# Optimization experiments

Hardware: AMD Instinct MI355X
Metric: run time of the kernel (lower is better)

## Reference

```python
import jax, jax.numpy as jnp
import numpy as np
import math

B, C, L_MIX, L_REF = 4, 512, 2048, 2048
NUM_HEADS = 8
HEAD_DIM = C // NUM_HEADS
MAX_LEN = 5000
EPS = 1e-5


def layer_norm(x, gamma, beta):
    mu = jnp.mean(x, axis=-1, keepdims=True)
    var = jnp.mean(jnp.square(x - mu), axis=-1, keepdims=True)
    return (x - mu) * jax.lax.rsqrt(var + EPS) * gamma + beta


def setup_inputs() -> dict:
    key = jax.random.key(0)
    ks = jax.random.split(key, 12)
    inp = {
        "query": jax.random.normal(ks[0], (B, C, L_MIX), dtype=jnp.float32),
        "key_value": jax.random.normal(ks[1], (B, C, L_REF), dtype=jnp.float32),
        "pos_encoding": jax.random.normal(ks[2], (1, MAX_LEN, C), dtype=jnp.float32) * 0.01,
        "q_gamma": jnp.ones((C,), jnp.float32),
        "q_beta": jnp.zeros((C,), jnp.float32),
        "k_gamma": jnp.ones((C,), jnp.float32),
        "k_beta": jnp.zeros((C,), jnp.float32),
        "Wq": jax.random.normal(ks[3], (C, C), jnp.float32) / math.sqrt(C),
        "bq": jax.random.normal(ks[4], (C,), jnp.float32) * 0.01,
        "Wk": jax.random.normal(ks[5], (C, C), jnp.float32) / math.sqrt(C),
        "bk": jax.random.normal(ks[6], (C,), jnp.float32) * 0.01,
        "Wv": jax.random.normal(ks[7], (C, C), jnp.float32) / math.sqrt(C),
        "bv": jax.random.normal(ks[8], (C,), jnp.float32) * 0.01,
        "Wo": jax.random.normal(ks[9], (C, C), jnp.float32) / math.sqrt(C),
        "bo": jax.random.normal(ks[10], (C,), jnp.float32) * 0.01,
    }
    return inp


def reference(query, key_value, pos_encoding, q_gamma, q_beta, k_gamma, k_beta,
              Wq, bq, Wk, bk, Wv, bv, Wo, bo):
    # (B, C, L) -> (B, L, C)
    q = jnp.transpose(query, (0, 2, 1))
    kv = jnp.transpose(key_value, (0, 2, 1))
    Lm, Lr = q.shape[1], kv.shape[1]
    q = q + pos_encoding[:, :Lm, :]
    kv = kv + pos_encoding[:, :Lr, :]
    q = layer_norm(q, q_gamma, q_beta)
    kv = layer_norm(kv, k_gamma, k_beta)
    Q = q @ Wq + bq          # (B, Lm, C)
    K = kv @ Wk + bk         # (B, Lr, C)
    V = kv @ Wv + bv         # (B, Lr, C)
    Q = Q.reshape(B, Lm, NUM_HEADS, HEAD_DIM)
    K = K.reshape(B, Lr, NUM_HEADS, HEAD_DIM)
    V = V.reshape(B, Lr, NUM_HEADS, HEAD_DIM)
    scale = math.sqrt(HEAD_DIM)
    scores = jnp.einsum('bqhd,bkhd->bhqk', Q, K) / scale  # (B, H, Lm, Lr)
    scores = jnp.clip(scores, -50.0, 50.0)
    attn = jax.nn.softmax(scores, axis=-1)  # dropout is identity at eval
    out = jnp.einsum('bhqk,bkhd->bqhd', attn, V).reshape(B, Lm, C)
    out = out @ Wo + bo
    out = out + q            # residual with normed/pos-encoded query, per source
    return jnp.transpose(out, (0, 2, 1))  # (B, C, Lm)
```

## Files before the change

### kernel.cpp

```cpp
#include <hip/hip_runtime.h>
#include <hip/hip_bf16.h>

#define B_ 4
#define C_ 512
#define L_ 2048
#define H_ 8
#define D_ 64
#define EPS_ 1e-5f

using short8 = __attribute__((ext_vector_type(8))) short;
using s4v    = __attribute__((ext_vector_type(4))) short;
using f32x4  = __attribute__((ext_vector_type(4))) float;

#if defined(__has_builtin)
#if __has_builtin(__builtin_amdgcn_exp2f)
#define EXP2(x) __builtin_amdgcn_exp2f(x)
#else
#define EXP2(x) exp2f(x)
#endif
#else
#define EXP2(x) exp2f(x)
#endif

#define GLOAD_LDS16(g, l)                                                     \
  __builtin_amdgcn_global_load_lds(                                           \
      (const __attribute__((address_space(1))) void*)(g),                     \
      (__attribute__((address_space(3))) void*)(l), 16, 0, 0)

static __device__ __forceinline__ short f2bf(float f) {
  __hip_bfloat16 h = __float2bfloat16(f);
  return __builtin_bit_cast(short, h);
}
static __device__ __forceinline__ float bf2f(short s) {
  return __bfloat162float(__builtin_bit_cast(__hip_bfloat16, s));
}

__global__ __launch_bounds__(256) void k_pre(
    const float* __restrict__ Wq, const float* __restrict__ Wk,
    const float* __restrict__ Wv, const float* __restrict__ Wo,
    short* __restrict__ Wt,
    const float* __restrict__ query, const float* __restrict__ kv,
    const float* __restrict__ pos,
    const float* __restrict__ qg, const float* __restrict__ qb,
    const float* __restrict__ kg, const float* __restrict__ kb,
    short* __restrict__ qn, short* __restrict__ kvn) {
  __shared__ alignas(16) float SB[16 * 516 + 32];
  int t = threadIdx.x;
  int id = blockIdx.x;

  if (id < 1024) {
    int m = id >> 8, rest = id & 255;
    int k0 = (rest >> 4) * 32, n0 = (rest & 15) * 32;
    const float* W = (m == 0) ? Wq : (m == 1) ? Wk : (m == 2) ? Wv : Wo;
    float (*T)[33] = (float(*)[33])SB;
    {
      int kl = t >> 3, n4 = (t & 7) * 4;
      float4 v = *(const float4*)(W + (size_t)(k0 + kl) * C_ + n0 + n4);
      T[kl][n4] = v.x; T[kl][n4 + 1] = v.y; T[kl][n4 + 2] = v.z; T[kl][n4 + 3] = v.w;
    }
    __syncthreads();
    {
      int nl = t >> 3, k4 = (t & 7) * 4;
      s4v o;
#pragma unroll
      for (int j = 0; j < 4; ++j) o[j] = f2bf(T[k4 + j][nl]);
      *(s4v*)(Wt + (size_t)(m * C_ + n0 + nl) * C_ + k0 + k4) = o;
    }
    return;
  }

  id -= 1024;
  int z  = id >> 9;
  int b  = (id >> 7) & 3;
  int l0 = (id & 127) * 16;
  const float* src = z ? kv : query;
  const float* g   = z ? kg : qg;
  const float* be  = z ? kb : qb;
  short* dst       = z ? kvn : qn;

  float (*T)[516] = (float(*)[516])SB;
  float* mu_s = SB + 16 * 516;
  float* rs_s = mu_s + 16;

#pragma unroll
  for (int i = 0; i < 8; ++i) {
    int idx = i * 256 + t;
    int cc = idx >> 2, lg = (idx & 3) * 4;
    float4 v = *(const float4*)(src + (size_t)(b * C_ + cc) * L_ + l0 + lg);
    T[lg + 0][cc] = v.x; T[lg + 1][cc] = v.y; T[lg + 2][cc] = v.z; T[lg + 3][cc] = v.w;
  }
  __syncthreads();
#pragma unroll
  for (int i = 0; i < 8; ++i) {
    int idx = i * 256 + t;
    int ll = idx >> 7, c4 = (idx & 127) * 4;
    float4 p = *(const float4*)(pos + (size_t)(l0 + ll) * C_ + c4);
    float4* tp = (float4*)&T[ll][c4];
    float4 cur = *tp;
    cur.x += p.x; cur.y += p.y; cur.z += p.z; cur.w += p.w;
    *tp = cur;
  }
  __syncthreads();
  {
    int row = t >> 4, j = t & 15;
    float s1 = 0.f, s2 = 0.f;
    for (int c = j; c < C_; c += 16) { float v = T[row][c]; s1 += v; s2 += v * v; }
    for (int m = 1; m < 16; m <<= 1) {
      s1 += __shfl_xor(s1, m, 64);
      s2 += __shfl_xor(s2, m, 64);
    }
    if (j == 0) {
      float mu  = s1 * (1.0f / C_);
      float var = s2 * (1.0f / C_) - mu * mu;
      mu_s[row] = mu;
      rs_s[row] = rsqrtf(var + EPS_);
    }
  }
  __syncthreads();
#pragma unroll
  for (int i = 0; i < 8; ++i) {
    int idx = i * 256 + t;
    int ll = idx >> 7, c4 = (idx & 127) * 4;
    float4 v  = *(const float4*)&T[ll][c4];
    float4 gv = *(const float4*)(g + c4);
    float4 bv = *(const float4*)(be + c4);
    float mu = mu_s[ll], rs = rs_s[ll];
    s4v o;
    o[0] = f2bf((v.x - mu) * rs * gv.x + bv.x);
    o[1] = f2bf((v.y - mu) * rs * gv.y + bv.y);
    o[2] = f2bf((v.z - mu) * rs * gv.z + bv.z);
    o[3] = f2bf((v.w - mu) * rs * gv.w + bv.w);
    *(s4v*)(dst + (size_t)(b * L_ + l0 + ll) * C_ + c4) = o;
  }
}

__global__ __launch_bounds__(256) void k_gemm_qkv(
    const short* __restrict__ qn, const short* __restrict__ kvn,
    const short* __restrict__ Wt,
    const float* __restrict__ bq, const float* __restrict__ bk, const float* __restrict__ bv,
    short* __restrict__ Qw, short* __restrict__ Kw, short* __restrict__ Vtg) {
  int z = blockIdx.z;
  const short* X    = z ? kvn : qn;
  const short* W    = Wt + (size_t)z * C_ * C_;
  const float* bias = (z == 0) ? bq : (z == 1) ? bk : bv;
  float sc          = (z == 0) ? 0.18033688f : 1.0f;

  int m0 = blockIdx.x * 128, n0 = blockIdx.y * 128;
  __shared__ alignas(16) short As[128 * 64];
  __shared__ alignas(16) short Bs[128 * 64];
  int t = threadIdx.x, lane = t & 63, w = t >> 6;
  int wm = w & 1, wn = w >> 1;
  int quad = lane >> 4, c = lane & 15;

  const short* Ag = X + (size_t)(m0 + w * 32 + (lane >> 3)) * C_ + (lane & 7) * 8;
  const short* Bg = W + (size_t)(n0 + w * 32 + (lane >> 3)) * C_ + (lane & 7) * 8;

  f32x4 zero4 = {0.f, 0.f, 0.f, 0.f};
  f32x4 acc[4][4];
  for (int i = 0; i < 4; ++i) for (int j = 0; j < 4; ++j) acc[i][j] = zero4;

  for (int k0 = 0; k0 < C_; k0 += 64) {
    __syncthreads();
#pragma unroll
    for (int j = 0; j < 4; ++j) {
      GLOAD_LDS16(Ag + (size_t)(j * 8) * C_ + k0, As + (w * 32 + j * 8) * 64);
      GLOAD_LDS16(Bg + (size_t)(j * 8) * C_ + k0, Bs + (w * 32 + j * 8) * 64);
    }
    __syncthreads();
#pragma unroll
    for (int kc = 0; kc < 2; ++kc) {
      short8 a[4], bf[4];
#pragma unroll
      for (int i = 0; i < 4; ++i)
        a[i]  = *(const short8*)(As + (wm * 64 + i * 16 + c) * 64 + kc * 32 + quad * 8);
#pragma unroll
      for (int j = 0; j < 4; ++j)
        bf[j] = *(const short8*)(Bs + (wn * 64 + j * 16 + c) * 64 + kc * 32 + quad * 8);
#pragma unroll
      for (int i = 0; i < 4; ++i)
#pragma unroll
        for (int j = 0; j < 4; ++j)
          acc[i][j] = __builtin_amdgcn_mfma_f32_16x16x32_bf16(a[i], bf[j], acc[i][j], 0, 0, 0);
    }
  }

  if (z == 2) {
#pragma unroll
    for (int i = 0; i < 4; ++i)
#pragma unroll
      for (int j = 0; j < 4; ++j) {
        int colg = n0 + wn * 64 + j * 16 + c;
        float bia = bias[colg];
        int hh = colg >> 6, dd = colg & 63;
        int rowg = m0 + wm * 64 + i * 16 + quad * 4;
        int bb = rowg >> 11, l = rowg & (L_ - 1);
        s4v o;
#pragma unroll
        for (int r = 0; r < 4; ++r) o[r] = f2bf(acc[i][j][r] + bia);
        *(s4v*)(Vtg + ((size_t)(bb * H_ + hh) * D_ + dd) * L_ + l) = o;
      }
  } else {
    short* Y = (z == 0) ? Qw : Kw;
#pragma unroll
    for (int i = 0; i < 4; ++i)
#pragma unroll
      for (int j = 0; j < 4; ++j) {
        int colg = n0 + wn * 64 + j * 16 + c;
        float bia = bias[colg];
        int rowg = m0 + wm * 64 + i * 16 + quad * 4;
#pragma unroll
        for (int r = 0; r < 4; ++r)
          Y[(size_t)(rowg + r) * C_ + colg] = f2bf((acc[i][j][r] + bia) * sc);
      }
  }
}

#define LDP 72
#define LDC 68
__global__ __launch_bounds__(256, 2) void k_attn(
    const short* __restrict__ Qw, const short* __restrict__ Kw,
    const short* __restrict__ Vtg, short* __restrict__ Ow) {
  int bh = blockIdx.x & 31;
  int l0 = (blockIdx.x >> 5) * 128;
  int b = bh >> 3, h = bh & 7;
  __shared__ alignas(16) short Pw[4][16 * LDP];
  __shared__ alignas(16) float Cbuf[128 * LDC];
  __shared__ float Lbuf[128];
  int t = threadIdx.x, lane = t & 63, w = t >> 6;
  int qh = w & 1, ls = w >> 1;
  int quad = lane >> 4, c = lane & 15;

  short8 qa[4][2];
#pragma unroll
  for (int s = 0; s < 4; ++s) {
    const short* qp = Qw + ((size_t)(b * L_ + l0 + qh * 64 + s * 16 + c) * H_ + h) * D_ + quad * 8;
    qa[s][0] = *(const short8*)qp;
    qa[s][1] = *(const short8*)(qp + 32);
  }

  f32x4 zero4 = {0.f, 0.f, 0.f, 0.f};
  f32x4 acc[4][4];
#pragma unroll
  for (int s = 0; s < 4; ++s)
    for (int dt = 0; dt < 4; ++dt) acc[s][dt] = zero4;
  float lsum[4] = {0.f, 0.f, 0.f, 0.f};

  const short* Kb = Kw + ((size_t)(b * L_) * H_ + h) * D_;
  const short* Vb = Vtg + (size_t)(b * H_ + h) * D_ * L_;
  short* pb = &Pw[w][0];

  for (int lr0 = ls * 64; lr0 < L_; lr0 += 128) {
    short8 kf[4][2], vf[4][2];
#pragma unroll
    for (int T = 0; T < 4; ++T) {
      const short* kp = Kb + (size_t)(lr0 + T * 16 + c) * C_ + quad * 8;
      kf[T][0] = *(const short8*)kp;
      kf[T][1] = *(const short8*)(kp + 32);
    }
#pragma unroll
    for (int dt = 0; dt < 4; ++dt) {
      const short* vp = Vb + (size_t)(dt * 16 + c) * L_ + lr0 + quad * 8;
      vf[dt][0] = *(const short8*)vp;
      vf[dt][1] = *(const short8*)(vp + 32);
    }

#pragma unroll
    for (int s = 0; s < 4; ++s) {
      f32x4 st[4] = {zero4, zero4, zero4, zero4};
#pragma unroll
      for (int T = 0; T < 4; ++T) {
        st[T] = __builtin_amdgcn_mfma_f32_16x16x32_bf16(kf[T][0], qa[s][0], st[T], 0, 0, 0);
        st[T] = __builtin_amdgcn_mfma_f32_16x16x32_bf16(kf[T][1], qa[s][1], st[T], 0, 0, 0);
      }
#pragma unroll
      for (int T = 0; T < 4; ++T) {
        s4v pk;
#pragma unroll
        for (int r = 0; r < 4; ++r) {
          float p = EXP2(st[T][r]);
          lsum[s] += p;
          pk[r] = f2bf(p);
        }
        *(s4v*)(pb + c * LDP + T * 16 + quad * 4) = pk;
      }
#pragma unroll
      for (int hf = 0; hf < 2; ++hf) {
        short8 pf = *(const short8*)(pb + c * LDP + hf * 32 + quad * 8);
#pragma unroll
        for (int dt = 0; dt < 4; ++dt)
          acc[s][dt] = __builtin_amdgcn_mfma_f32_16x16x32_bf16(vf[dt][hf], pf, acc[s][dt], 0, 0, 0);
      }
    }
  }

#pragma unroll
  for (int s = 0; s < 4; ++s) {
    lsum[s] += __shfl_xor(lsum[s], 16, 64);
    lsum[s] += __shfl_xor(lsum[s], 32, 64);
  }

  if (ls == 1) {
#pragma unroll
    for (int s = 0; s < 4; ++s) {
      int q = qh * 64 + s * 16 + c;
#pragma unroll
      for (int dt = 0; dt < 4; ++dt)
        *(f32x4*)(Cbuf + q * LDC + dt * 16 + quad * 4) = acc[s][dt];
      if (quad == 0) Lbuf[q] = lsum[s];
    }
  }
  __syncthreads();
  if (ls == 0) {
#pragma unroll
    for (int s = 0; s < 4; ++s) {
      int q = qh * 64 + s * 16 + c;
      float inv = 1.0f / (lsum[s] + Lbuf[q]);
#pragma unroll
      for (int dt = 0; dt < 4; ++dt) {
        f32x4 o = *(const f32x4*)(Cbuf + q * LDC + dt * 16 + quad * 4);
        s4v ov;
#pragma unroll
        for (int r = 0; r < 4; ++r) ov[r] = f2bf((acc[s][dt][r] + o[r]) * inv);
        *(s4v*)(Ow + ((size_t)(b * L_ + l0 + q) * H_ + h) * D_ + dt * 16 + quad * 4) = ov;
      }
    }
  }
}

__global__ __launch_bounds__(256) void k_gemm_out(
    const short* __restrict__ Ow, const short* __restrict__ Wot,
    const float* __restrict__ bo, const short* __restrict__ qn,
    float* __restrict__ out) {
  int m0 = blockIdx.x * 128, n0 = blockIdx.y * 128;
  __shared__ alignas(16) short As[128 * 64];
  __shared__ alignas(16) short Bs[128 * 64];
  int t = threadIdx.x, lane = t & 63, w = t >> 6;
  int wm = w & 1, wn = w >> 1;
  int quad = lane >> 4, c = lane & 15;

  const short* Ag = Ow  + (size_t)(m0 + w * 32 + (lane >> 3)) * C_ + (lane & 7) * 8;
  const short* Bg = Wot + (size_t)(n0 + w * 32 + (lane >> 3)) * C_ + (lane & 7) * 8;

  f32x4 zero4 = {0.f, 0.f, 0.f, 0.f};
  f32x4 acc[4][4];
  for (int i = 0; i < 4; ++i) for (int j = 0; j < 4; ++j) acc[i][j] = zero4;

  for (int k0 = 0; k0 < C_; k0 += 64) {
    __syncthreads();
#pragma unroll
    for (int j = 0; j < 4; ++j) {
      GLOAD_LDS16(Ag + (size_t)(j * 8) * C_ + k0, As + (w * 32 + j * 8) * 64);
      GLOAD_LDS16(Bg + (size_t)(j * 8) * C_ + k0, Bs + (w * 32 + j * 8) * 64);
    }
    __syncthreads();
#pragma unroll
    for (int kc = 0; kc < 2; ++kc) {
      short8 a[4], bf[4];
#pragma unroll
      for (int i = 0; i < 4; ++i)
        a[i]  = *(const short8*)(As + (wm * 64 + i * 16 + c) * 64 + kc * 32 + quad * 8);
#pragma unroll
      for (int j = 0; j < 4; ++j)
        bf[j] = *(const short8*)(Bs + (wn * 64 + j * 16 + c) * 64 + kc * 32 + quad * 8);
#pragma unroll
      for (int i = 0; i < 4; ++i)
#pragma unroll
        for (int j = 0; j < 4; ++j)
          acc[i][j] = __builtin_amdgcn_mfma_f32_16x16x32_bf16(a[i], bf[j], acc[i][j], 0, 0, 0);
    }
  }

  int bb = m0 >> 11;
#pragma unroll
  for (int i = 0; i < 4; ++i)
#pragma unroll
    for (int j = 0; j < 4; ++j) {
      int colg = n0 + wn * 64 + j * 16 + c;
      float bia = bo[colg];
      int rowg = m0 + wm * 64 + i * 16 + quad * 4;
      int l = rowg & (L_ - 1);
      float4 vv;
      float* pv = &vv.x;
#pragma unroll
      for (int r = 0; r < 4; ++r)
        pv[r] = acc[i][j][r] + bia + bf2f(qn[(size_t)(rowg + r) * C_ + colg]);
      *(float4*)(out + ((size_t)bb * C_ + colg) * L_ + l) = vv;
    }
}

extern "C" void kernel_launch(void* const* d_in, const int* in_sizes, int n_in,
                              void* d_out, int out_size, void* d_ws, size_t ws_size,
                              hipStream_t stream) {
  const float* query     = (const float*)d_in[0];
  const float* key_value = (const float*)d_in[1];
  const float* pos       = (const float*)d_in[2];
  const float* qg        = (const float*)d_in[3];
  const float* qb        = (const float*)d_in[4];
  const float* kg        = (const float*)d_in[5];
  const float* kb        = (const float*)d_in[6];
  const float* Wq        = (const float*)d_in[7];
  const float* bq        = (const float*)d_in[8];
  const float* Wk        = (const float*)d_in[9];
  const float* bk        = (const float*)d_in[10];
  const float* Wv        = (const float*)d_in[11];
  const float* bv        = (const float*)d_in[12];
  const float* Wo        = (const float*)d_in[13];
  const float* bo        = (const float*)d_in[14];
  float* out = (float*)d_out;

  char* ws = (char*)d_ws;
  const size_t SZ = (size_t)B_ * L_ * C_ * 2;
  short* qn  = (short*)(ws + 0 * SZ);
  short* kvn = (short*)(ws + 1 * SZ);
  short* Qw  = (short*)(ws + 2 * SZ);
  short* Kw  = (short*)(ws + 3 * SZ);
  short* Vtg = (short*)(ws + 4 * SZ);
  short* Ow  = (short*)(ws + 5 * SZ);
  short* Wt  = (short*)(ws + 6 * SZ);

  k_pre<<<dim3(3072), 256, 0, stream>>>(Wq, Wk, Wv, Wo, Wt,
                                        query, key_value, pos, qg, qb, kg, kb, qn, kvn);
  k_gemm_qkv<<<dim3(8192 / 128, C_ / 128, 3), 256, 0, stream>>>(qn, kvn, Wt, bq, bk, bv, Qw, Kw, Vtg);
  k_attn<<<dim3(512), 256, 0, stream>>>(Qw, Kw, Vtg, Ow);
  k_gemm_out<<<dim3(8192 / 128, C_ / 128, 1), 256, 0, stream>>>(Ow, Wt + (size_t)3 * C_ * C_, bo, qn, out);
}
```

Measured before the change: 235.5 us.

## Split attention key range four ways per block and shrink query tile

Each attention block now handles 64 queries instead of 128, and its four waves each take a quarter of the key range rather than a 2x2 query/key split. Partial outputs and row sums are reduced through shared memory in three serialized steps. Grid size doubles and launch bounds ask for four blocks per CU, to raise occupancy and parallelism. In exchange, every K/V tile is loaded for half as many queries, which doubles K/V traffic per query, and the extra reduction barriers add overhead.

```diff
diff --git a/kernel.cpp b/kernel.cpp
--- a/kernel.cpp
+++ b/kernel.cpp
@@ -217,23 +217,22 @@
 
 #define LDP 72
 #define LDC 68
-__global__ __launch_bounds__(256, 2) void k_attn(
+__global__ __launch_bounds__(256, 4) void k_attn(
     const short* __restrict__ Qw, const short* __restrict__ Kw,
     const short* __restrict__ Vtg, short* __restrict__ Ow) {
   int bh = blockIdx.x & 31;
-  int l0 = (blockIdx.x >> 5) * 128;
+  int l0 = (blockIdx.x >> 5) * 64;
   int b = bh >> 3, h = bh & 7;
   __shared__ alignas(16) short Pw[4][16 * LDP];
-  __shared__ alignas(16) float Cbuf[128 * LDC];
-  __shared__ float Lbuf[128];
+  __shared__ alignas(16) float Cbuf[64 * LDC];
+  __shared__ float Lbuf[64];
   int t = threadIdx.x, lane = t & 63, w = t >> 6;
-  int qh = w & 1, ls = w >> 1;
   int quad = lane >> 4, c = lane & 15;
 
   short8 qa[4][2];
 #pragma unroll
   for (int s = 0; s < 4; ++s) {
-    const short* qp = Qw + ((size_t)(b * L_ + l0 + qh * 64 + s * 16 + c) * H_ + h) * D_ + quad * 8;
+    const short* qp = Qw + ((size_t)(b * L_ + l0 + s * 16 + c) * H_ + h) * D_ + quad * 8;
     qa[s][0] = *(const short8*)qp;
     qa[s][1] = *(const short8*)(qp + 32);
   }
@@ -249,7 +248,7 @@
   const short* Vb = Vtg + (size_t)(b * H_ + h) * D_ * L_;
   short* pb = &Pw[w][0];
 
-  for (int lr0 = ls * 64; lr0 < L_; lr0 += 128) {
+  for (int lr0 = w * 64; lr0 < L_; lr0 += 256) {
     short8 kf[4][2], vf[4][2];
 #pragma unroll
     for (int T = 0; T < 4; ++T) {
@@ -299,10 +298,10 @@
     lsum[s] += __shfl_xor(lsum[s], 32, 64);
   }
 
-  if (ls == 1) {
+  if (w == 3) {
 #pragma unroll
     for (int s = 0; s < 4; ++s) {
-      int q = qh * 64 + s * 16 + c;
+      int q = s * 16 + c;
 #pragma unroll
       for (int dt = 0; dt < 4; ++dt)
         *(f32x4*)(Cbuf + q * LDC + dt * 16 + quad * 4) = acc[s][dt];
@@ -310,10 +309,44 @@
     }
   }
   __syncthreads();
-  if (ls == 0) {
+  if (w == 2 || w == 1) {
+    if (w == 2) {
+#pragma unroll
+      for (int s = 0; s < 4; ++s) {
+        int q = s * 16 + c;
+#pragma unroll
+        for (int dt = 0; dt < 4; ++dt) {
+          f32x4* p = (f32x4*)(Cbuf + q * LDC + dt * 16 + quad * 4);
+          f32x4 o = *p;
+#pragma unroll
+          for (int r = 0; r < 4; ++r) o[r] += acc[s][dt][r];
+          *p = o;
+        }
+        if (quad == 0) Lbuf[q] += lsum[s];
+      }
+    }
+  }
+  __syncthreads();
+  if (w == 1) {
 #pragma unroll
     for (int s = 0; s < 4; ++s) {
-      int q = qh * 64 + s * 16 + c;
+      int q = s * 16 + c;
+#pragma unroll
+      for (int dt = 0; dt < 4; ++dt) {
+        f32x4* p = (f32x4*)(Cbuf + q * LDC + dt * 16 + quad * 4);
+        f32x4 o = *p;
+#pragma unroll
+        for (int r = 0; r < 4; ++r) o[r] += acc[s][dt][r];
+        *p = o;
+      }
+      if (quad == 0) Lbuf[q] += lsum[s];
+    }
+  }
+  __syncthreads();
+  if (w == 0) {
+#pragma unroll
+    for (int s = 0; s < 4; ++s) {
+      int q = s * 16 + c;
       float inv = 1.0f / (lsum[s] + Lbuf[q]);
 #pragma unroll
       for (int dt = 0; dt < 4; ++dt) {
@@ -421,6 +454,6 @@
   k_pre<<<dim3(3072), 256, 0, stream>>>(Wq, Wk, Wv, Wo, Wt,
                                         query, key_value, pos, qg, qb, kg, kb, qn, kvn);
   k_gemm_qkv<<<dim3(8192 / 128, C_ / 128, 3), 256, 0, stream>>>(qn, kvn, Wt, bq, bk, bv, Qw, Kw, Vtg);
-  k_attn<<<dim3(512), 256, 0, stream>>>(Qw, Kw, Vtg, Ow);
+  k_attn<<<dim3(1024), 256, 0, stream>>>(Qw, Kw, Vtg, Ow);
   k_gemm_out<<<dim3(8192 / 128, C_ / 128, 1), 256, 0, stream>>>(Ow, Wt + (size_t)3 * C_ * C_, bo, qn, out);
 }
```

Result: slower. 521.1 us (+121.3%).
